# Kernel tuning notes

Hardware: AMD Instinct MI355X
Metric: run time of the kernel (lower is better)

Reference implementation:

```python
import jax, jax.numpy as jnp
import numpy as np

ENTRY_SIZE = 8192
TUPLE_SIZE = 16
N_NEURONS = ENTRY_SIZE // TUPLE_SIZE            # 512
ADDR_SPACE = 2 ** TUPLE_SIZE                     # 65536
BATCH = 4096


def setup_inputs() -> dict:
    key = jax.random.key(0)
    k1, k2, k3 = jax.random.split(key, 3)
    # Binary input bits [B, entry_size]
    inp = jax.random.randint(k1, (BATCH, ENTRY_SIZE), 0, 2, dtype=jnp.int32)
    # Permutation mapping bits -> tuples (identity permutation; arange fill)
    tuple_mapping = jnp.arange(ENTRY_SIZE, dtype=jnp.int64)
    # Dense RAM tables emulating the per-neuron dicts:
    #   counts[n, a] = number of training samples that hit address a in neuron n
    #                  (0 means the address was never trained -> not in dict)
    #   sums[n, a]   = accumulated target sum for that address
    counts = jax.random.randint(k2, (N_NEURONS, ADDR_SPACE), 0, 4, dtype=jnp.int32)
    sums = jax.random.normal(k3, (N_NEURONS, ADDR_SPACE), dtype=jnp.float32)
    return {"input": inp, "tuple_mapping": tuple_mapping, "counts": counts, "sums": sums}


def reference(input, tuple_mapping, counts, sums):
    """RegressionWisard.predict with centrality='mean'.

    input:  [B, entry_size] binary bits (int32)
    tuple_mapping: [entry_size] permutation (int)
    counts: [n_neurons, 2^tuple_size] int32 RAM hit counts
    sums:   [n_neurons, 2^tuple_size] float32 RAM target sums
    """
    B = input.shape[0]
    # Map and group bits into tuples: [B, N, T]
    mapped = jnp.take(input, tuple_mapping, axis=1).reshape(B, N_NEURONS, TUPLE_SIZE)
    # Binary address per (sample, neuron); tidx flips so bit 0 is the MSB.
    pow2 = (jnp.int32(1) << jnp.arange(TUPLE_SIZE - 1, -1, -1, dtype=jnp.int32))
    addr = jnp.einsum("bnt,t->bn", mapped, pow2)  # [B, N], values in [0, 2^T)
    neuron_idx = jnp.arange(N_NEURONS, dtype=jnp.int32)[None, :]  # [1, N]
    c = counts[neuron_idx, addr]  # [B, N]
    s = sums[neuron_idx, addr]    # [B, N]
    trained = c > 0               # dict-membership (torch.isin) equivalent
    response = jnp.sum(jnp.where(trained, s, jnp.float32(0)), axis=1)      # [B]
    counters = jnp.sum(jnp.where(trained, c, 0), axis=1).astype(s.dtype)   # [B]
    return jnp.nan_to_num(response / counters)
```

## Files before the change

kernel.cpp:

```cpp
#include <hip/hip_runtime.h>


constexpr int BATCH   = 4096;
constexpr int ENTRY   = 8192;
constexpr int TUP     = 16;
constexpr int NEUR    = ENTRY / TUP;
constexpr int THREADS = 256;
constexpr int SPB     = 2;

__global__ __launch_bounds__(THREADS) void wisard_kernel(
    const int*   __restrict__ input,
    const int*   __restrict__ mapping,
    const int*   __restrict__ counts,
    const float* __restrict__ sums,
    float*       __restrict__ out)
{
    __shared__ unsigned int packed[SPB][ENTRY / 32];
    __shared__ float s_resp[SPB][THREADS / 64];
    __shared__ int   s_cnt [SPB][THREADS / 64];

    const int tid  = threadIdx.x;
    const int lane = tid & 63;
    const int wv   = tid >> 6;
    const int b0   = blockIdx.x * SPB;

    #pragma unroll
    for (int s = 0; s < SPB; ++s) {
        const int* row = input + (size_t)(b0 + s) * ENTRY;
        #pragma unroll
        for (int i = wv; i < ENTRY / 64; i += THREADS / 64) {
            const int v = __builtin_nontemporal_load(&row[i * 64 + lane]);
            const unsigned long long m = __ballot(v & 1);
            if (lane == 0) {
                packed[s][i * 2]     = (unsigned int)(m);
                packed[s][i * 2 + 1] = (unsigned int)(m >> 32);
            }
        }
    }
    __syncthreads();

    int idx[SPB][2];
    #pragma unroll
    for (int k = 0; k < 2; ++k) {
        const int n = tid + k * THREADS;
        const int* map_n = mapping + n * TUP;
        int addr[SPB] = {0, 0};
        #pragma unroll
        for (int t = 0; t < TUP; ++t) {
            const int j = map_n[t];
            const unsigned w = j >> 5, sh = j & 31;
            #pragma unroll
            for (int s = 0; s < SPB; ++s) {
                const int bit = (packed[s][w] >> sh) & 1;
                addr[s] = (addr[s] << 1) | bit;
            }
        }
        #pragma unroll
        for (int s = 0; s < SPB; ++s) idx[s][k] = (n << 16) | addr[s];
    }

    int   cv[SPB][2];
    float sv[SPB][2];
    #pragma unroll
    for (int s = 0; s < SPB; ++s)
        #pragma unroll
        for (int k = 0; k < 2; ++k) {
            cv[s][k] = counts[idx[s][k]];
            sv[s][k] = sums  [idx[s][k]];
        }

    float resp[SPB];
    int   cnt [SPB];
    #pragma unroll
    for (int s = 0; s < SPB; ++s) {
        resp[s] = 0.0f; cnt[s] = 0;
        #pragma unroll
        for (int k = 0; k < 2; ++k) {
            const bool t = cv[s][k] > 0;
            resp[s] += t ? sv[s][k] : 0.0f;
            cnt [s] += t ? cv[s][k] : 0;
        }
    }

    #pragma unroll
    for (int s = 0; s < SPB; ++s) {
        float r = resp[s]; int c = cnt[s];
        #pragma unroll
        for (int off = 32; off > 0; off >>= 1) {
            r += __shfl_down(r, off, 64);
            c += __shfl_down(c, off, 64);
        }
        if (lane == 0) { s_resp[s][wv] = r; s_cnt[s][wv] = c; }
    }
    __syncthreads();
    if (tid < SPB) {
        float r = 0.0f; int c = 0;
        #pragma unroll
        for (int w = 0; w < THREADS / 64; ++w) { r += s_resp[tid][w]; c += s_cnt[tid][w]; }
        out[b0 + tid] = (c > 0) ? (r / (float)c) : 0.0f;
    }
}

extern "C" void kernel_launch(void* const* d_in, const int* in_sizes, int n_in,
                              void* d_out, int out_size, void* d_ws, size_t ws_size,
                              hipStream_t stream) {
    (void)in_sizes; (void)n_in; (void)out_size; (void)d_ws; (void)ws_size;
    const int*   input   = (const int*)d_in[0];
    const int*   mapping = (const int*)d_in[1];
    const int*   counts  = (const int*)d_in[2];
    const float* sums    = (const float*)d_in[3];
    float*       out     = (float*)d_out;

    wisard_kernel<<<BATCH / SPB, THREADS, 0, stream>>>(input, mapping, counts, sums, out);
}
```

Baseline: 367.0 us.

## Read tuple bits directly with vector loads instead of packing to LDS

Drops the shared-memory bit-packing stage and its block barrier. When a neuron's mapping is 16 contiguous, aligned indices, each thread reads its 16 input ints with four 128-bit loads and builds the address in registers. Other mappings fall back to per-element gathers from global memory. Input reads become per-thread strided vector loads rather than coalesced wave loads, and each thread first reads 16 mapping entries to decide which path to take.

```diff
diff --git a/kernel.cpp b/kernel.cpp
--- a/kernel.cpp
+++ b/kernel.cpp
@@ -7,6 +7,9 @@
 constexpr int NEUR    = ENTRY / TUP;
 constexpr int THREADS = 256;
 constexpr int SPB     = 2;
+constexpr int KPT     = NEUR / THREADS;
+
+typedef int v4i __attribute__((ext_vector_type(4)));
 
 __global__ __launch_bounds__(THREADS) void wisard_kernel(
     const int*   __restrict__ input,
@@ -15,7 +18,6 @@
     const float* __restrict__ sums,
     float*       __restrict__ out)
 {
-    __shared__ unsigned int packed[SPB][ENTRY / 32];
     __shared__ float s_resp[SPB][THREADS / 64];
     __shared__ int   s_cnt [SPB][THREADS / 64];
 
@@ -24,50 +26,56 @@
     const int wv   = tid >> 6;
     const int b0   = blockIdx.x * SPB;
 
+    int   cv[SPB][KPT];
+    float sv[SPB][KPT];
+
     #pragma unroll
-    for (int s = 0; s < SPB; ++s) {
-        const int* row = input + (size_t)(b0 + s) * ENTRY;
+    for (int k = 0; k < KPT; ++k) {
+        const int n = tid + k * THREADS;
+        const int* map_n = mapping + n * TUP;
+
+        const int m0 = map_n[0];
+        bool contig = ((m0 & 3) == 0);
         #pragma unroll
-        for (int i = wv; i < ENTRY / 64; i += THREADS / 64) {
-            const int v = __builtin_nontemporal_load(&row[i * 64 + lane]);
-            const unsigned long long m = __ballot(v & 1);
-            if (lane == 0) {
-                packed[s][i * 2]     = (unsigned int)(m);
-                packed[s][i * 2 + 1] = (unsigned int)(m >> 32);
+        for (int t = 1; t < TUP; ++t) contig &= (map_n[t] == m0 + t);
+
+        int addr[SPB];
+        if (contig) {
+            #pragma unroll
+            for (int s = 0; s < SPB; ++s) {
+                const v4i* p = reinterpret_cast<const v4i*>(
+                    input + (size_t)(b0 + s) * ENTRY + m0);
+                const v4i w0 = __builtin_nontemporal_load(p);
+                const v4i w1 = __builtin_nontemporal_load(p + 1);
+                const v4i w2 = __builtin_nontemporal_load(p + 2);
+                const v4i w3 = __builtin_nontemporal_load(p + 3);
+                addr[s] = ((w0.x & 1) << 15) | ((w0.y & 1) << 14)
+                        | ((w0.z & 1) << 13) | ((w0.w & 1) << 12)
+                        | ((w1.x & 1) << 11) | ((w1.y & 1) << 10)
+                        | ((w1.z & 1) <<  9) | ((w1.w & 1) <<  8)
+                        | ((w2.x & 1) <<  7) | ((w2.y & 1) <<  6)
+                        | ((w2.z & 1) <<  5) | ((w2.w & 1) <<  4)
+                        | ((w3.x & 1) <<  3) | ((w3.y & 1) <<  2)
+                        | ((w3.z & 1) <<  1) |  (w3.w & 1);
+            }
+        } else {
+            #pragma unroll
+            for (int s = 0; s < SPB; ++s) {
+                const int* row = input + (size_t)(b0 + s) * ENTRY;
+                int a = 0;
+                #pragma unroll
+                for (int t = 0; t < TUP; ++t) a = (a << 1) | (row[map_n[t]] & 1);
+                addr[s] = a;
             }
         }
+
+        #pragma unroll
+        for (int s = 0; s < SPB; ++s) {
+            const size_t idx = ((size_t)n << 16) | (unsigned)addr[s];
+            cv[s][k] = counts[idx];
+            sv[s][k] = sums  [idx];
+        }
     }
-    __syncthreads();
-
-    int idx[SPB][2];
-    #pragma unroll
-    for (int k = 0; k < 2; ++k) {
-        const int n = tid + k * THREADS;
-        const int* map_n = mapping + n * TUP;
-        int addr[SPB] = {0, 0};
-        #pragma unroll
-        for (int t = 0; t < TUP; ++t) {
-            const int j = map_n[t];
-            const unsigned w = j >> 5, sh = j & 31;
-            #pragma unroll
-            for (int s = 0; s < SPB; ++s) {
-                const int bit = (packed[s][w] >> sh) & 1;
-                addr[s] = (addr[s] << 1) | bit;
-            }
-        }
-        #pragma unroll
-        for (int s = 0; s < SPB; ++s) idx[s][k] = (n << 16) | addr[s];
-    }
-
-    int   cv[SPB][2];
-    float sv[SPB][2];
-    #pragma unroll
-    for (int s = 0; s < SPB; ++s)
-        #pragma unroll
-        for (int k = 0; k < 2; ++k) {
-            cv[s][k] = counts[idx[s][k]];
-            sv[s][k] = sums  [idx[s][k]];
-        }
 
     float resp[SPB];
     int   cnt [SPB];
@@ -75,10 +83,10 @@
     for (int s = 0; s < SPB; ++s) {
         resp[s] = 0.0f; cnt[s] = 0;
         #pragma unroll
-        for (int k = 0; k < 2; ++k) {
-            const bool t = cv[s][k] > 0;
-            resp[s] += t ? sv[s][k] : 0.0f;
-            cnt [s] += t ? cv[s][k] : 0;
+        for (int k = 0; k < KPT; ++k) {
+            const bool tr = cv[s][k] > 0;
+            resp[s] += tr ? sv[s][k] : 0.0f;
+            cnt [s] += tr ? cv[s][k] : 0;
         }
     }
 
```

Result: no change. 365.4 us (-0.5%).
